# Optimization experiments

Hardware: AMD Instinct MI355X
Metric: run time of the kernel (lower is better)

Reference implementation:

```python
import jax, jax.numpy as jnp
import numpy as np
import math

B, S, D = 8, 1024, 1024
NH, NKV, HD = 16, 8, 64
BLK_NUM, BLK_SIZE = 128, 8

def apply_rope(x, cos, sin):
    # x: (B,S,H,HD); cos/sin: (S, HD//2)
    x1 = x[..., 0::2]
    x2 = x[..., 1::2]
    c = cos[None, :, None, :]
    s = sin[None, :, None, :]
    r1 = x1 * c - x2 * s
    r2 = x1 * s + x2 * c
    out = jnp.stack([r1, r2], axis=-1).reshape(x.shape)
    return out

def setup_inputs() -> dict:
    key = jax.random.key(0)
    ks = jax.random.split(key, 7)
    x = jax.random.normal(ks[0], (B, S, D), dtype=jnp.float32)
    scale = 1.0 / math.sqrt(D)
    wq = jax.random.normal(ks[1], (D, NH * HD), dtype=jnp.float32) * scale
    wk = jax.random.normal(ks[2], (D, NKV * HD), dtype=jnp.float32) * scale
    wv = jax.random.normal(ks[3], (D, NKV * HD), dtype=jnp.float32) * scale
    wo = jax.random.normal(ks[4], (NH * HD, D), dtype=jnp.float32) * scale
    pos = jnp.arange(S, dtype=jnp.float32)
    inv_freq = 1.0 / (10000.0 ** (jnp.arange(0, HD, 2, dtype=jnp.float32) / HD))
    ang = pos[:, None] * inv_freq[None, :]
    freqs_cis_cos = jnp.cos(ang)
    freqs_cis_sin = jnp.sin(ang)
    return {"x": x, "wq": wq, "wk": wk, "wv": wv, "wo": wo,
            "freqs_cis_cos": freqs_cis_cos, "freqs_cis_sin": freqs_cis_sin,
            "start_pos": 0}

def reference(x, wq, wk, wv, wo, freqs_cis_cos, freqs_cis_sin, start_pos):
    q = (x @ wq).reshape(B, S, NH, HD)
    k = (x @ wk).reshape(B, S, NKV, HD)
    v = (x @ wv).reshape(B, S, NKV, HD)
    q = apply_rope(q, freqs_cis_cos, freqs_cis_sin)
    k = apply_rope(k, freqs_cis_cos, freqs_cis_sin)
    # GQA: repeat kv heads
    rep = NH // NKV
    k = jnp.repeat(k, rep, axis=2)  # (B,S,NH,HD)
    v = jnp.repeat(v, rep, axis=2)
    # block-causal mask: q in block i attends to kv blocks j <= i
    blk_id = jnp.arange(S) // BLK_SIZE
    mask = blk_id[:, None] >= blk_id[None, :]  # (S,S)
    scores = jnp.einsum('bqhd,bkhd->bhqk', q, k) / math.sqrt(HD)
    scores = jnp.where(mask[None, None], scores, -jnp.inf)
    attn = jax.nn.softmax(scores, axis=-1)
    out = jnp.einsum('bhqk,bkhd->bqhd', attn, v).reshape(B, S, NH * HD)
    return out @ wo
```

## Files before the change

### kernel.cpp

```cpp
#include <hip/hip_runtime.h>
#include <cstdint>
#include <math.h>

#define B_   8
#define S_   1024
#define D_   1024
#define NH_  16
#define NKV_ 8
#define HD_  64
#define M_   (B_*S_)

using bf16   = __bf16;
using bf16x4 = __attribute__((ext_vector_type(4))) __bf16;
using bf16x8 = __attribute__((ext_vector_type(8))) __bf16;
using f32x4  = __attribute__((ext_vector_type(4))) float;

__device__ __forceinline__ void gll16(const bf16* g, const bf16* l) {
    __builtin_amdgcn_global_load_lds(
        (const __attribute__((address_space(1))) unsigned int*)(uintptr_t)g,
        (__attribute__((address_space(3))) unsigned int*)(uintptr_t)l,
        16, 0, 0);
}

__device__ __forceinline__ void dsr128(bf16x8& d, const bf16* p) {
    asm volatile("ds_read_b128 %0, %1" : "=v"(d) : "v"((unsigned)(uintptr_t)p));
}
__device__ __forceinline__ void lgkm0() {
    asm volatile("s_waitcnt lgkmcnt(0)" ::: "memory");
    __builtin_amdgcn_sched_barrier(0);
}
__device__ __forceinline__ void vm_wait0()  { asm volatile("s_waitcnt vmcnt(0)"  ::: "memory"); }
__device__ __forceinline__ void vm_wait4()  { asm volatile("s_waitcnt vmcnt(4)"  ::: "memory"); }
__device__ __forceinline__ void vm_wait8()  { asm volatile("s_waitcnt vmcnt(8)"  ::: "memory"); }
__device__ __forceinline__ void bar()       { __builtin_amdgcn_s_barrier(); asm volatile("" ::: "memory"); }

__global__ void k_prep1(const float* __restrict__ x,
                        const float* __restrict__ wq, const float* __restrict__ wk,
                        const float* __restrict__ wv, const float* __restrict__ wo,
                        bf16* __restrict__ xb, bf16* __restrict__ wqkvT, bf16* __restrict__ woT) {
    __shared__ float tile[64 * 65];
    int bid = blockIdx.x;
    int t = threadIdx.x;
    if (bid < 8192) {
        int i = bid * 256 + t;
        float4 v = ((const float4*)x)[i];
        bf16x4 o = { (bf16)v.x, (bf16)v.y, (bf16)v.z, (bf16)v.w };
        ((bf16x4*)xb)[i] = o;
        return;
    }
    int b2 = bid - 8192;
    int bx = b2 % 48, by = b2 / 48;
    const int R = 1024;
    const float* in; bf16* out; int C, xo;
    if (bx < 16)      { in = wq; out = wqkvT;               C = 1024; xo = bx; }
    else if (bx < 24) { in = wk; out = wqkvT + 1024 * 1024; C = 512;  xo = bx - 16; }
    else if (bx < 32) { in = wv; out = wqkvT + 1536 * 1024; C = 512;  xo = bx - 24; }
    else              { in = wo; out = woT;                 C = 1024; xo = bx - 32; }
    int r0 = by * 64, c0 = xo * 64;
    #pragma unroll
    for (int it = 0; it < 16; ++it) {
        int idx = it * 256 + t;
        int r = idx >> 6, c = idx & 63;
        tile[r * 65 + c] = in[(size_t)(r0 + r) * C + c0 + c];
    }
    __syncthreads();
    #pragma unroll
    for (int it = 0; it < 16; ++it) {
        int idx = it * 256 + t;
        int c = idx >> 6, r = idx & 63;
        out[(size_t)(c0 + c) * R + r0 + r] = (bf16)tile[r * 65 + c];
    }
}

template <typename OutT>
__global__ __launch_bounds__(256, 2) void k_gemm128(const bf16* __restrict__ A,
                                                    const bf16* __restrict__ Bt,
                                                    OutT* __restrict__ C, int M, int N, int K) {
    __shared__ __align__(16) bf16 aL2[2 * 128 * 64];
    __shared__ __align__(16) bf16 bL2[2 * 128 * 64];
    const int t    = threadIdx.x;
    const int lane = t & 63;
    const int w    = t >> 6;
    const int quad = lane >> 4;
    const int l16  = lane & 15;
    const int wr   = w >> 1;
    const int wc   = w & 1;

    int bid = blockIdx.y * gridDim.x + blockIdx.x;
    int cpx = (gridDim.x * gridDim.y) >> 3;
    int sw  = (bid & 7) * cpx + (bid >> 3);
    int bx  = sw % gridDim.x, by = sw / gridDim.x;
    const int m0 = by * 128;
    const int n0 = bx * 128;

    f32x4 acc[4][4] = {};

    auto stage = [&](int kb, int sb) {
        const int k0 = kb << 6;
        #pragma unroll
        for (int it = 0; it < 4; ++it) {
            int ci = it * 256 + t;
            int r = ci >> 3, c = ci & 7;
            int cg = c ^ (r & 7);
            gll16(A + (size_t)(m0 + r) * K + k0 + cg * 8, aL2 + sb * 8192 + ci * 8);
        }
        #pragma unroll
        for (int it = 0; it < 4; ++it) {
            int ci = it * 256 + t;
            int r = ci >> 3, c = ci & 7;
            int cg = c ^ (r & 7);
            gll16(Bt + (size_t)(n0 + r) * K + k0 + cg * 8, bL2 + sb * 8192 + ci * 8);
        }
    };

    const int NT = K >> 6;

    auto tileStep = [&](int T, int buf) {
        if (T + 1 < NT) { stage(T + 1, buf ^ 1); vm_wait8(); }
        else vm_wait0();
        bar();
        const bf16* aL = aL2 + buf * 8192;
        const bf16* bL = bL2 + buf * 8192;
        #pragma unroll
        for (int kk = 0; kk < 2; ++kk) {
            bf16x8 af[4], bfr[4];
            #pragma unroll
            for (int mi = 0; mi < 4; ++mi) {
                int row = wr * 64 + mi * 16 + l16;
                int ch  = (kk * 4 + quad) ^ (row & 7);
                af[mi] = *(const bf16x8*)&aL[row * 64 + ch * 8];
            }
            #pragma unroll
            for (int ni = 0; ni < 4; ++ni) {
                int row = wc * 64 + ni * 16 + l16;
                int ch  = (kk * 4 + quad) ^ (row & 7);
                bfr[ni] = *(const bf16x8*)&bL[row * 64 + ch * 8];
            }
            __builtin_amdgcn_s_setprio(1);
            #pragma unroll
            for (int mi = 0; mi < 4; ++mi)
                #pragma unroll
                for (int ni = 0; ni < 4; ++ni)
                    acc[mi][ni] = __builtin_amdgcn_mfma_f32_16x16x32_bf16(af[mi], bfr[ni], acc[mi][ni], 0, 0, 0);
            __builtin_amdgcn_s_setprio(0);
        }
        bar();
    };

    stage(0, 0);
    for (int T = 0; T < NT; T += 2) {
        tileStep(T, 0);
        tileStep(T + 1, 1);
    }

    #pragma unroll
    for (int mi = 0; mi < 4; ++mi)
        #pragma unroll
        for (int ni = 0; ni < 4; ++ni)
            #pragma unroll
            for (int r = 0; r < 4; ++r) {
                int row = m0 + wr * 64 + mi * 16 + quad * 4 + r;
                int col = n0 + wc * 64 + ni * 16 + l16;
                C[(size_t)row * N + col] = (OutT)acc[mi][ni][r];
            }
}

__global__ void k_prep2(const bf16* __restrict__ qkv, const float* __restrict__ cosg,
                        const float* __restrict__ sing, bf16* __restrict__ qd,
                        bf16* __restrict__ kd, bf16* __restrict__ vt) {
    __shared__ __align__(16) bf16 tile[64 * 72];
    int bid = blockIdx.x;
    int t = threadIdx.x;
    if (bid < 8192) {
        if (t < 192) {
            int token = bid;
            int b = token >> 10, s = token & 1023;
            int hh = t >> 3, i8 = t & 7;
            float4 c4 = *(const float4*)&cosg[s * 32 + i8 * 4];
            float4 s4 = *(const float4*)&sing[s * 32 + i8 * 4];
            int srcBase, dstBase;
            bf16* dst;
            float sf;
            if (hh < 16) {
                srcBase = token * 2048 + hh * 64;
                dstBase = ((b * NH_ + hh) * S_ + s) * 64;
                dst = qd;
                sf = 0.180336879f;
            } else {
                int h = hh - 16;
                srcBase = token * 2048 + 1024 + h * 64;
                dstBase = ((b * NKV_ + h) * S_ + s) * 64;
                dst = kd;
                sf = 1.0f;
            }
            bf16x8 v = *(const bf16x8*)&qkv[srcBase + i8 * 8];
            const float cc[4] = { c4.x, c4.y, c4.z, c4.w };
            const float ss[4] = { s4.x, s4.y, s4.z, s4.w };
            bf16x8 o;
            #pragma unroll
            for (int j = 0; j < 4; ++j) {
                float e  = (float)v[2 * j];
                float od = (float)v[2 * j + 1];
                o[2 * j]     = (bf16)(sf * (e * cc[j] - od * ss[j]));
                o[2 * j + 1] = (bf16)(sf * (e * ss[j] + od * cc[j]));
            }
            *(bf16x8*)&dst[dstBase + i8 * 8] = o;
        }
        return;
    }
    int b2 = bid - 8192;
    int st = b2 & 15;
    int h  = (b2 >> 4) & 7;
    int b  = b2 >> 7;
    int s0 = st * 64;
    #pragma unroll
    for (int it = 0; it < 2; ++it) {
        int ci = it * 256 + t;
        int r = ci >> 3, c = ci & 7;
        *(uint4*)&tile[r * 72 + c * 8] =
            *(const uint4*)&qkv[(size_t)(b * S_ + s0 + r) * 2048 + 1536 + h * 64 + c * 8];
    }
    __syncthreads();
    #pragma unroll
    for (int it = 0; it < 2; ++it) {
        int ci = it * 256 + t;
        int d = ci >> 3, sc = ci & 7;
        int g = sc >> 2, q4 = sc & 3;
        bf16x8 v;
        #pragma unroll
        for (int j = 0; j < 8; ++j) {
            int s_ext = g * 32 + q4 * 4 + (j & 3) + 16 * (j >> 2);
            v[j] = tile[s_ext * 72 + d];
        }
        *(bf16x8*)&vt[(size_t)((b * NKV_ + h) * 64 + d) * S_ + s0 + sc * 8] = v;
    }
}

__global__ __launch_bounds__(256, 4) void k_attn(const bf16* __restrict__ q, const bf16* __restrict__ k,
                                                 const bf16* __restrict__ vt, bf16* __restrict__ out) {
    __shared__ __align__(16) bf16 kt[2 * 64 * 64];
    __shared__ __align__(16) bf16 vtt[2 * 64 * 64];
    int bid = blockIdx.x;
    int qt = 15 - (bid >> 7);
    int combo = bid & 127;
    int b = combo >> 4, h = combo & 15;
    int hkv = h >> 1;
    int t = threadIdx.x;
    int w = t >> 6, lane = t & 63, quad = lane >> 4, l16 = lane & 15;

    const bf16* qh = q + (size_t)(b * NH_ + h) * S_ * 64;
    int qw = qt * 64 + w * 16;
    const bf16* qb = qh + (size_t)(qw + l16) * 64;
    bf16x8 qf0 = *(const bf16x8*)(qb + quad * 8);
    bf16x8 qf1 = *(const bf16x8*)(qb + 32 + quad * 8);

    const bf16* kg = k  + (size_t)(b * NKV_ + hkv) * S_ * 64;
    const bf16* vg = vt + (size_t)(b * NKV_ + hkv) * 64 * S_;

    const int sr0 = t >> 3;
    const int cs  = t & 7;

    auto stage = [&](int u, int buf) {
        int k0 = u * 64;
        #pragma unroll
        for (int it = 0; it < 2; ++it) {
            int r  = sr0 + it * 32;
            int cg = cs ^ (r & 7);
            int ci = it * 256 + t;
            gll16(kg + (size_t)(k0 + r) * 64 + cg * 8, kt  + buf * 4096 + ci * 8);
            gll16(vg + (size_t)r * S_ + k0 + cg * 8,   vtt + buf * 4096 + ci * 8);
        }
    };

    const bf16 one = (bf16)1.0f;
    const bf16x8 vones = { one, one, one, one, one, one, one, one };

    f32x4 o[4] = {};
    f32x4 ol = {};
    const int klim = ((qw + l16) & ~7) + 8;

    auto unit = [&](const bf16* ktb, const bf16* vtb, int k0, bool diag) {
        bf16x8 af[8];
        #pragma unroll
        for (int kk = 0; kk < 2; ++kk)
            #pragma unroll
            for (int f = 0; f < 4; ++f) {
                int row = f * 16 + l16;
                int ch  = (kk * 4 + quad) ^ (row & 7);
                dsr128(af[kk * 4 + f], &ktb[row * 64 + ch * 8]);
            }
        lgkm0();
        f32x4 sc[4] = {};
        __builtin_amdgcn_s_setprio(1);
        #pragma unroll
        for (int kk = 0; kk < 2; ++kk)
            #pragma unroll
            for (int f = 0; f < 4; ++f)
                sc[f] = __builtin_amdgcn_mfma_f32_16x16x32_bf16(af[kk * 4 + f], kk ? qf1 : qf0, sc[f], 0, 0, 0);
        __builtin_amdgcn_s_setprio(0);

        bf16x8 vbf[8];
        #pragma unroll
        for (int dc = 0; dc < 4; ++dc)
            #pragma unroll
            for (int kk = 0; kk < 2; ++kk) {
                int row = dc * 16 + l16;
                int ch  = (kk * 4 + quad) ^ (row & 7);
                dsr128(vbf[dc * 2 + kk], &vtb[row * 64 + ch * 8]);
            }

        float p[4][4];
        #pragma unroll
        for (int f = 0; f < 4; ++f)
            #pragma unroll
            for (int r = 0; r < 4; ++r) {
                float pv = __builtin_amdgcn_exp2f(sc[f][r]);
                if (diag && (k0 + f * 16 + quad * 4 + r >= klim)) pv = 0.f;
                p[f][r] = pv;
            }
        bf16x8 pa0, pa1;
        #pragma unroll
        for (int j = 0; j < 4; ++j) {
            pa0[j]     = (bf16)p[0][j];
            pa0[j + 4] = (bf16)p[1][j];
            pa1[j]     = (bf16)p[2][j];
            pa1[j + 4] = (bf16)p[3][j];
        }
        ol = __builtin_amdgcn_mfma_f32_16x16x32_bf16(pa0, vones, ol, 0, 0, 0);
        ol = __builtin_amdgcn_mfma_f32_16x16x32_bf16(pa1, vones, ol, 0, 0, 0);

        lgkm0();
        __builtin_amdgcn_s_setprio(1);
        #pragma unroll
        for (int dc = 0; dc < 4; ++dc)
            #pragma unroll
            for (int kk = 0; kk < 2; ++kk)
                o[dc] = __builtin_amdgcn_mfma_f32_16x16x32_bf16(kk ? pa1 : pa0, vbf[dc * 2 + kk], o[dc], 0, 0, 0);
        __builtin_amdgcn_s_setprio(0);
    };

    const int NU = qt + 1;
    stage(0, 0);
    asm volatile("" :: "v"(qf0), "v"(qf1));

    int u = 0;
    for (; u + 2 <= NU; u += 2) {
        bar();
        stage(u + 1, 1);
        vm_wait4();
        bar();
        unit(kt, vtt, u * 64, false);
        bar();
        bool hn = (u + 2 < NU);
        if (hn) { stage(u + 2, 0); vm_wait4(); } else vm_wait0();
        bar();
        unit(kt + 4096, vtt + 4096, (u + 1) * 64, (u + 1) == NU - 1);
    }
    if (u < NU) {
        bar();
        vm_wait0();
        bar();
        unit(kt, vtt, u * 64, true);
    }

    #pragma unroll
    for (int r = 0; r < 4; ++r) {
        float invl = 1.0f / ol[r];
        #pragma unroll
        for (int dc = 0; dc < 4; ++dc) {
            int row = qw + quad * 4 + r;
            int col = h * 64 + dc * 16 + l16;
            out[(size_t)(b * S_ + row) * 1024 + col] = (bf16)(o[dc][r] * invl);
        }
    }
}

extern "C" void kernel_launch(void* const* d_in, const int* in_sizes, int n_in,
                              void* d_out, int out_size, void* d_ws, size_t ws_size,
                              hipStream_t stream) {
    const float* x  = (const float*)d_in[0];
    const float* wq = (const float*)d_in[1];
    const float* wk = (const float*)d_in[2];
    const float* wv = (const float*)d_in[3];
    const float* wo = (const float*)d_in[4];
    const float* fc = (const float*)d_in[5];
    const float* fs = (const float*)d_in[6];
    (void)in_sizes; (void)n_in; (void)out_size; (void)ws_size;

    char* ws = (char*)d_ws;
    bf16* xb    = (bf16*)(ws);
    bf16* wqkvT = (bf16*)(ws + (16u << 20));
    bf16* woT   = (bf16*)(ws + (20u << 20));
    bf16* qkvb  = (bf16*)(ws + (22u << 20));
    bf16* kb    = (bf16*)(ws + (54u << 20));
    bf16* vtb   = (bf16*)(ws + (62u << 20));
    bf16* qb    = xb;
    bf16* attnb = qkvb;

    k_prep1<<<dim3(8960), dim3(256), 0, stream>>>(x, wq, wk, wv, wo, xb, wqkvT, woT);

    k_gemm128<bf16><<<dim3(16, 64), dim3(256), 0, stream>>>(xb, wqkvT, qkvb, M_, 2048, 1024);

    k_prep2<<<dim3(9216), dim3(256), 0, stream>>>(qkvb, fc, fs, qb, kb, vtb);

    k_attn<<<dim3(2048), dim3(256), 0, stream>>>(qb, kb, vtb, attnb);

    k_gemm128<float><<<dim3(8, 64), dim3(256), 0, stream>>>(attnb, woT, (float*)d_out, M_, 1024, 1024);
}
```

Baseline: 190.9 us.

## Process both GQA query heads per block to share K/V tiles

Each attention workgroup now handles the two query heads that share one KV head, so every staged K/V tile in LDS is used for two score and PV computations. This halves global K/V traffic and LDS staging per query head, and halves the grid size. In exchange it roughly doubles accumulator and fragment register use per thread, and the V fragment loads are split into two halves to limit register pressure. With the grid halved, occupancy and load balance across CUs may drop.

```diff
diff --git a/kernel.cpp b/kernel.cpp
--- a/kernel.cpp
+++ b/kernel.cpp
@@ -241,18 +241,20 @@
     __shared__ __align__(16) bf16 kt[2 * 64 * 64];
     __shared__ __align__(16) bf16 vtt[2 * 64 * 64];
     int bid = blockIdx.x;
-    int qt = 15 - (bid >> 7);
-    int combo = bid & 127;
-    int b = combo >> 4, h = combo & 15;
-    int hkv = h >> 1;
+    int qt = 15 - (bid >> 6);
+    int combo = bid & 63;
+    int b = combo >> 3, hkv = combo & 7;
+    int hA = hkv * 2, hB = hkv * 2 + 1;
     int t = threadIdx.x;
     int w = t >> 6, lane = t & 63, quad = lane >> 4, l16 = lane & 15;
 
-    const bf16* qh = q + (size_t)(b * NH_ + h) * S_ * 64;
     int qw = qt * 64 + w * 16;
-    const bf16* qb = qh + (size_t)(qw + l16) * 64;
-    bf16x8 qf0 = *(const bf16x8*)(qb + quad * 8);
-    bf16x8 qf1 = *(const bf16x8*)(qb + 32 + quad * 8);
+    const bf16* qhA = q + (size_t)(b * NH_ + hA) * S_ * 64 + (size_t)(qw + l16) * 64;
+    const bf16* qhB = q + (size_t)(b * NH_ + hB) * S_ * 64 + (size_t)(qw + l16) * 64;
+    bf16x8 qfA0 = *(const bf16x8*)(qhA + quad * 8);
+    bf16x8 qfA1 = *(const bf16x8*)(qhA + 32 + quad * 8);
+    bf16x8 qfB0 = *(const bf16x8*)(qhB + quad * 8);
+    bf16x8 qfB1 = *(const bf16x8*)(qhB + 32 + quad * 8);
 
     const bf16* kg = k  + (size_t)(b * NKV_ + hkv) * S_ * 64;
     const bf16* vg = vt + (size_t)(b * NKV_ + hkv) * 64 * S_;
@@ -275,8 +277,8 @@
     const bf16 one = (bf16)1.0f;
     const bf16x8 vones = { one, one, one, one, one, one, one, one };
 
-    f32x4 o[4] = {};
-    f32x4 ol = {};
+    f32x4 oA[4] = {}, oB[4] = {};
+    f32x4 olA = {}, olB = {};
     const int klim = ((qw + l16) & ~7) + 8;
 
     auto unit = [&](const bf16* ktb, const bf16* vtb, int k0, bool diag) {
@@ -290,58 +292,103 @@
                 dsr128(af[kk * 4 + f], &ktb[row * 64 + ch * 8]);
             }
         lgkm0();
-        f32x4 sc[4] = {};
+        f32x4 scA[4] = {}, scB[4] = {};
         __builtin_amdgcn_s_setprio(1);
         #pragma unroll
         for (int kk = 0; kk < 2; ++kk)
             #pragma unroll
             for (int f = 0; f < 4; ++f)
-                sc[f] = __builtin_amdgcn_mfma_f32_16x16x32_bf16(af[kk * 4 + f], kk ? qf1 : qf0, sc[f], 0, 0, 0);
+                scA[f] = __builtin_amdgcn_mfma_f32_16x16x32_bf16(af[kk * 4 + f], kk ? qfA1 : qfA0, scA[f], 0, 0, 0);
+        #pragma unroll
+        for (int kk = 0; kk < 2; ++kk)
+            #pragma unroll
+            for (int f = 0; f < 4; ++f)
+                scB[f] = __builtin_amdgcn_mfma_f32_16x16x32_bf16(af[kk * 4 + f], kk ? qfB1 : qfB0, scB[f], 0, 0, 0);
         __builtin_amdgcn_s_setprio(0);
 
-        bf16x8 vbf[8];
-        #pragma unroll
-        for (int dc = 0; dc < 4; ++dc)
+        bf16x8 vb1[4];
+        #pragma unroll
+        for (int dc = 0; dc < 2; ++dc)
             #pragma unroll
             for (int kk = 0; kk < 2; ++kk) {
                 int row = dc * 16 + l16;
                 int ch  = (kk * 4 + quad) ^ (row & 7);
-                dsr128(vbf[dc * 2 + kk], &vtb[row * 64 + ch * 8]);
+                dsr128(vb1[dc * 2 + kk], &vtb[row * 64 + ch * 8]);
             }
 
         float p[4][4];
+        bf16x8 paA0, paA1, paB0, paB1;
         #pragma unroll
         for (int f = 0; f < 4; ++f)
             #pragma unroll
             for (int r = 0; r < 4; ++r) {
-                float pv = __builtin_amdgcn_exp2f(sc[f][r]);
+                float pv = __builtin_amdgcn_exp2f(scA[f][r]);
                 if (diag && (k0 + f * 16 + quad * 4 + r >= klim)) pv = 0.f;
                 p[f][r] = pv;
             }
-        bf16x8 pa0, pa1;
         #pragma unroll
         for (int j = 0; j < 4; ++j) {
-            pa0[j]     = (bf16)p[0][j];
-            pa0[j + 4] = (bf16)p[1][j];
-            pa1[j]     = (bf16)p[2][j];
-            pa1[j + 4] = (bf16)p[3][j];
-        }
-        ol = __builtin_amdgcn_mfma_f32_16x16x32_bf16(pa0, vones, ol, 0, 0, 0);
-        ol = __builtin_amdgcn_mfma_f32_16x16x32_bf16(pa1, vones, ol, 0, 0, 0);
+            paA0[j]     = (bf16)p[0][j];
+            paA0[j + 4] = (bf16)p[1][j];
+            paA1[j]     = (bf16)p[2][j];
+            paA1[j + 4] = (bf16)p[3][j];
+        }
+        olA = __builtin_amdgcn_mfma_f32_16x16x32_bf16(paA0, vones, olA, 0, 0, 0);
+        olA = __builtin_amdgcn_mfma_f32_16x16x32_bf16(paA1, vones, olA, 0, 0, 0);
+
+        #pragma unroll
+        for (int f = 0; f < 4; ++f)
+            #pragma unroll
+            for (int r = 0; r < 4; ++r) {
+                float pv = __builtin_amdgcn_exp2f(scB[f][r]);
+                if (diag && (k0 + f * 16 + quad * 4 + r >= klim)) pv = 0.f;
+                p[f][r] = pv;
+            }
+        #pragma unroll
+        for (int j = 0; j < 4; ++j) {
+            paB0[j]     = (bf16)p[0][j];
+            paB0[j + 4] = (bf16)p[1][j];
+            paB1[j]     = (bf16)p[2][j];
+            paB1[j + 4] = (bf16)p[3][j];
+        }
+        olB = __builtin_amdgcn_mfma_f32_16x16x32_bf16(paB0, vones, olB, 0, 0, 0);
+        olB = __builtin_amdgcn_mfma_f32_16x16x32_bf16(paB1, vones, olB, 0, 0, 0);
 
         lgkm0();
         __builtin_amdgcn_s_setprio(1);
         #pragma unroll
-        for (int dc = 0; dc < 4; ++dc)
-            #pragma unroll
-            for (int kk = 0; kk < 2; ++kk)
-                o[dc] = __builtin_amdgcn_mfma_f32_16x16x32_bf16(kk ? pa1 : pa0, vbf[dc * 2 + kk], o[dc], 0, 0, 0);
+        for (int dc = 0; dc < 2; ++dc)
+            #pragma unroll
+            for (int kk = 0; kk < 2; ++kk) {
+                oA[dc] = __builtin_amdgcn_mfma_f32_16x16x32_bf16(kk ? paA1 : paA0, vb1[dc * 2 + kk], oA[dc], 0, 0, 0);
+                oB[dc] = __builtin_amdgcn_mfma_f32_16x16x32_bf16(kk ? paB1 : paB0, vb1[dc * 2 + kk], oB[dc], 0, 0, 0);
+            }
+        __builtin_amdgcn_s_setprio(0);
+
+        bf16x8 vb2[4];
+        #pragma unroll
+        for (int dc = 0; dc < 2; ++dc)
+            #pragma unroll
+            for (int kk = 0; kk < 2; ++kk) {
+                int row = (dc + 2) * 16 + l16;
+                int ch  = (kk * 4 + quad) ^ (row & 7);
+                dsr128(vb2[dc * 2 + kk], &vtb[row * 64 + ch * 8]);
+            }
+        lgkm0();
+        __builtin_amdgcn_s_setprio(1);
+        #pragma unroll
+        for (int dc = 0; dc < 2; ++dc)
+            #pragma unroll
+            for (int kk = 0; kk < 2; ++kk) {
+                oA[dc + 2] = __builtin_amdgcn_mfma_f32_16x16x32_bf16(kk ? paA1 : paA0, vb2[dc * 2 + kk], oA[dc + 2], 0, 0, 0);
+                oB[dc + 2] = __builtin_amdgcn_mfma_f32_16x16x32_bf16(kk ? paB1 : paB0, vb2[dc * 2 + kk], oB[dc + 2], 0, 0, 0);
+            }
         __builtin_amdgcn_s_setprio(0);
     };
 
     const int NU = qt + 1;
     stage(0, 0);
-    asm volatile("" :: "v"(qf0), "v"(qf1));
+    asm volatile("" :: "v"(qfA0), "v"(qfA1), "v"(qfB0), "v"(qfB1));
 
     int u = 0;
     for (; u + 2 <= NU; u += 2) {
@@ -365,12 +412,13 @@
 
     #pragma unroll
     for (int r = 0; r < 4; ++r) {
-        float invl = 1.0f / ol[r];
+        float invA = 1.0f / olA[r];
+        float invB = 1.0f / olB[r];
+        int row = qw + quad * 4 + r;
         #pragma unroll
         for (int dc = 0; dc < 4; ++dc) {
-            int row = qw + quad * 4 + r;
-            int col = h * 64 + dc * 16 + l16;
-            out[(size_t)(b * S_ + row) * 1024 + col] = (bf16)(o[dc][r] * invl);
+            out[(size_t)(b * S_ + row) * 1024 + hA * 64 + dc * 16 + l16] = (bf16)(oA[dc][r] * invA);
+            out[(size_t)(b * S_ + row) * 1024 + hB * 64 + dc * 16 + l16] = (bf16)(oB[dc][r] * invB);
         }
     }
 }
@@ -403,7 +451,7 @@
 
     k_prep2<<<dim3(9216), dim3(256), 0, stream>>>(qkvb, fc, fs, qb, kb, vtb);
 
-    k_attn<<<dim3(2048), dim3(256), 0, stream>>>(qb, kb, vtb, attnb);
+    k_attn<<<dim3(1024), dim3(256), 0, stream>>>(qb, kb, vtb, attnb);
 
     k_gemm128<float><<<dim3(8, 64), dim3(256), 0, stream>>>(attnb, woT, (float*)d_out, M_, 1024, 1024);
 }
```

Measured after the change: 216.9 us. 1.14x slower.
